# Optimization experiments

Hardware: AMD Instinct MI355X
Metric: run time of the kernel (lower is better)

The kernel has to match this reference:

```python
import jax, jax.numpy as jnp
import numpy as np

B, N, C = 8, 1025, 1024
H = 8
D = C // H  # 128
LORA = 16
TOK = 1024

def setup_inputs() -> dict:
    key = jax.random.key(0)
    ks = jax.random.split(key, 16)
    s = 0.02
    return {
        "x": jax.random.normal(ks[0], (B, N, C), jnp.float32),
        "style_k": jax.random.normal(ks[1], (B, N, C), jnp.float32),
        "style_v": jax.random.normal(ks[2], (B, N, C), jnp.float32),
        "W_qkv": jax.random.normal(ks[3], (C, 3 * C), jnp.float32) * s,
        "W_proj": jax.random.normal(ks[4], (C, C), jnp.float32) * s,
        "b_proj": jnp.zeros((C,), jnp.float32),
        "ak": jax.random.normal(ks[5], (TOK, LORA), jnp.float32) * s,
        "bk": jax.random.normal(ks[6], (LORA, C), jnp.float32) * s,
        "av": jax.random.normal(ks[7], (TOK, LORA), jnp.float32) * s,
        "bv": jax.random.normal(ks[8], (LORA, C), jnp.float32) * s,
        "W1": jax.random.normal(ks[9], (C, C // 4), jnp.float32) * s,
        "b1": jnp.zeros((C // 4,), jnp.float32),
        "W2": jax.random.normal(ks[10], (C // 4, 1), jnp.float32) * s,
        "b2": jnp.zeros((1,), jnp.float32),
    }

def reference(x, style_k, style_v, W_qkv, W_proj, b_proj, ak, bk, av, bv, W1, b1, W2, b2):
    Bx, Nx, Cx = x.shape
    # cls-token gating MLP over transposed patch tokens: cp has shape [B, C, N-1], N-1 == C
    cls_token = x[:, :1, :]                         # [B,1,C]
    cp = jnp.transpose(x[:, 1:, :], (0, 2, 1))      # [B,C,N-1]
    h = jax.nn.relu(cp @ W1 + b1)                   # [B,C,C//4]
    attn_w = jax.nn.sigmoid(h @ W2 + b2)            # [B,C,1]
    attn_w = attn_w[..., 0][:, None, :]             # [B,1,C]
    weighted_cls = cls_token * attn_w               # [B,1,C]

    qkv = (x @ W_qkv).reshape(Bx, Nx, 3, H, D)
    q, k, v = qkv[:, :, 0], qkv[:, :, 1], qkv[:, :, 2]  # each [B,N,H,D]

    tokens_k = ak @ bk                              # [TOK, C] (TOK == C)
    tokens_v = av @ bv
    lora_k = (style_k @ tokens_k.T).reshape(Bx, Nx, H, D)
    lora_v = (style_v @ tokens_v.T).reshape(Bx, Nx, H, D)

    kk = k + lora_k
    vv = v + lora_v
    scale = D ** -0.5  # xformers default softmax scale
    scores = jnp.einsum('bqhd,bkhd->bhqk', q, kk) * scale
    attn = jax.nn.softmax(scores, axis=-1)
    out = jnp.einsum('bhqk,bkhd->bqhd', attn, vv).reshape(Bx, Nx, Cx)
    out = out @ W_proj + b_proj

    x_return = jnp.concatenate([out[:, :1, :] + weighted_cls, out[:, 1:, :]], axis=1)
    return (x_return, vv)
```

## Files before the change

kernel.cpp:

```cpp
#include <hip/hip_runtime.h>
#include <hip/hip_bf16.h>
#include <stdint.h>

#define B_ 8
#define N_ 1025
#define C_ 1024
#define H_ 8
#define D_ 128
#define TOK_ 1024
#define LORA_ 16
#define M_ 8200
#define NPAD_ 1032

using bf16x8 = __attribute__((ext_vector_type(8))) short;
using f32x4  = __attribute__((ext_vector_type(4))) float;
typedef unsigned short u16;

__device__ __forceinline__ u16 f2bf(float f) {
    union { float f; unsigned u; } v; v.f = f;
    unsigned r = v.u + 0x7fffu + ((v.u >> 16) & 1u);
    return (u16)(r >> 16);
}

__device__ __forceinline__ void gload16(const u16* g, u16* l) {
    __builtin_amdgcn_global_load_lds(
        (const __attribute__((address_space(1))) void*)g,
        (__attribute__((address_space(3))) void*)l, 16, 0, 0);
}

__device__ __forceinline__ int xcd_swz(int bid, int nwg) {
    int cpx = nwg >> 3;
    return (bid & 7) * cpx + (bid >> 3);
}

__global__ __launch_bounds__(256) void cast3_kernel(
    const float* __restrict__ x, const float* __restrict__ sk, const float* __restrict__ sv,
    u16* __restrict__ xb, u16* __restrict__ skb, u16* __restrict__ svb)
{
    const float* in = blockIdx.y == 0 ? x : (blockIdx.y == 1 ? sk : sv);
    u16* out = blockIdx.y == 0 ? xb : (blockIdx.y == 1 ? skb : svb);
    size_t i = (size_t)blockIdx.x * 256 + threadIdx.x;
    float4 a = *((const float4*)in + i * 2);
    float4 b = *((const float4*)in + i * 2 + 1);
    bf16x8 v;
    v[0] = (short)f2bf(a.x); v[1] = (short)f2bf(a.y);
    v[2] = (short)f2bf(a.z); v[3] = (short)f2bf(a.w);
    v[4] = (short)f2bf(b.x); v[5] = (short)f2bf(b.y);
    v[6] = (short)f2bf(b.z); v[7] = (short)f2bf(b.w);
    *(bf16x8*)(out + i * 8) = v;
}

__global__ __launch_bounds__(256) void padcast16_kernel(
    const float* __restrict__ ak, const float* __restrict__ av,
    u16* __restrict__ akp, u16* __restrict__ avp)
{
    const float* in = blockIdx.y ? av : ak;
    u16* out = blockIdx.y ? avp : akp;
    int i = blockIdx.x * 256 + threadIdx.x;
    int t = i >> 4, l = i & 15;
    out[(size_t)t * 32 + l] = f2bf(in[i]);
    out[(size_t)t * 32 + 16 + l] = 0;
}

__global__ __launch_bounds__(256) void castb_kernel(
    const float* __restrict__ bk, const float* __restrict__ bv,
    u16* __restrict__ bkb, u16* __restrict__ bvb)
{
    const float* in = blockIdx.y ? bv : bk;
    u16* out = blockIdx.y ? bvb : bkb;
    int i = blockIdx.x * 256 + threadIdx.x;
    out[i] = f2bf(in[i]);
}

__global__ __launch_bounds__(256) void lora16_mfma(
    const u16* __restrict__ skb, const u16* __restrict__ svb,
    const u16* __restrict__ bkb, const u16* __restrict__ bvb,
    u16* __restrict__ sk16p, u16* __restrict__ sv16p)
{
    const u16* sb = blockIdx.y ? svb : skb;
    const u16* bb = blockIdx.y ? bvb : bkb;
    u16* op = blockIdx.y ? sv16p : sk16p;
    const int lane = threadIdx.x & 63, wid = threadIdx.x >> 6;
    const int base = blockIdx.x * 64 + wid * 16;
    int ma = base + (lane & 15); if (ma > M_ - 1) ma = M_ - 1;
    const int l = lane & 15;
    const u16* arow = sb + (size_t)ma * C_ + (lane >> 4) * 8;
    const u16* brow = bb + (size_t)l * C_ + (lane >> 4) * 8;
    f32x4 acc = {0.f, 0.f, 0.f, 0.f};
#pragma unroll
    for (int k0 = 0; k0 < C_; k0 += 32) {
        bf16x8 af = *(const bf16x8*)(arow + k0);
        bf16x8 bf = *(const bf16x8*)(brow + k0);
        acc = __builtin_amdgcn_mfma_f32_16x16x32_bf16(af, bf, acc, 0, 0, 0);
    }
#pragma unroll
    for (int r = 0; r < 4; ++r) {
        int m = base + (lane >> 4) * 4 + r; if (m > M_ - 1) m = M_ - 1;
        op[(size_t)m * 32 + l] = f2bf(acc[r]);
        op[(size_t)m * 32 + 16 + l] = 0;
    }
}

__global__ __launch_bounds__(256) void wt_kernel(
    const float* __restrict__ in, u16* __restrict__ out, int K, int Nw)
{
    __shared__ float t[32][33];
    int n0 = blockIdx.x * 32, k0 = blockIdx.y * 32;
    int tx = threadIdx.x & 31, ty = threadIdx.x >> 5;
#pragma unroll
    for (int yy = 0; yy < 32; yy += 8)
        t[ty + yy][tx] = in[(size_t)(k0 + ty + yy) * Nw + n0 + tx];
    __syncthreads();
#pragma unroll
    for (int yy = 0; yy < 32; yy += 8)
        out[(size_t)(n0 + ty + yy) * K + k0 + tx] = f2bf(t[tx][ty + yy]);
}

__global__ __launch_bounds__(256) void xt_kernel(
    const float* __restrict__ x, u16* __restrict__ xT)
{
    __shared__ float tb[32][33];
    int t0 = blockIdx.x * 32, c0 = blockIdx.y * 32, b = blockIdx.z;
    int tx = threadIdx.x & 31, ty = threadIdx.x >> 5;
#pragma unroll
    for (int yy = 0; yy < 32; yy += 8)
        tb[ty + yy][tx] = x[((size_t)b * N_ + 1 + t0 + ty + yy) * C_ + c0 + tx];
    __syncthreads();
#pragma unroll
    for (int yy = 0; yy < 32; yy += 8)
        xT[((size_t)b * 1024 + c0 + ty + yy) * 1024 + t0 + tx] = f2bf(tb[tx][ty + yy]);
}

__global__ __launch_bounds__(256) void vvt_kernel(
    const float* __restrict__ vv, u16* __restrict__ vvT)
{
    __shared__ float t[32][33];
    int n0 = blockIdx.x * 32, d0 = blockIdx.y * 32, bh = blockIdx.z;
    int b = bh >> 3, h = bh & 7;
    int tx = threadIdx.x & 31, ty = threadIdx.x >> 5;
#pragma unroll
    for (int yy = 0; yy < 32; yy += 8) {
        int n = n0 + ty + yy; if (n > 1024) n = 1024;
        t[ty + yy][tx] = vv[((size_t)(b * N_) + n) * C_ + h * D_ + d0 + tx];
    }
    __syncthreads();
#pragma unroll
    for (int yy = 0; yy < 32; yy += 8) {
        int n = n0 + tx;
        if (n < NPAD_)
            vvT[((size_t)bh * D_ + d0 + ty + yy) * NPAD_ + n] = f2bf(t[tx][ty + yy]);
    }
}

__device__ __forceinline__ void stage_tile(
    const u16* __restrict__ base, int row0, int maxrow,
    u16* lds, int k0, int lane, int wid)
{
#pragma unroll
    for (int j = 0; j < 4; ++j) {
        int i = wid * 4 + j;
        int p = i * 1024 + 16 * lane;
        int row = p >> 7, cb = p & 127;
        int cbs = cb ^ ((row & 7) << 4);
        int gr = row0 + row; if (gr > maxrow) gr = maxrow;
        gload16(base + (size_t)gr * 1024 + k0 + (cbs >> 1), lds + i * 512);
    }
}

__device__ __forceinline__ void gemm_pass(
    const u16* __restrict__ A, const u16* __restrict__ Bt, int row0, int nb0,
    u16* As, u16* Bs, f32x4 acc[4][4],
    const int lane, const int wid, const int wr, const int wc)
{
    for (int k0 = 0; k0 < 1024; k0 += 64) {
        __syncthreads();
        stage_tile(A,  row0, M_ - 1,    As, k0, lane, wid);
        stage_tile(Bt, nb0,  (1 << 30), Bs, k0, lane, wid);
        __syncthreads();
#pragma unroll
        for (int ks = 0; ks < 2; ++ks) {
            bf16x8 af[4], bfr[4];
#pragma unroll
            for (int mi = 0; mi < 4; ++mi) {
                int r = wr * 64 + mi * 16 + (lane & 15);
                int byte = (r * 128 + ks * 64 + (lane >> 4) * 16) ^ ((r & 7) << 4);
                af[mi] = *(const bf16x8*)((const char*)As + byte);
            }
#pragma unroll
            for (int ni = 0; ni < 4; ++ni) {
                int r = wc * 64 + ni * 16 + (lane & 15);
                int byte = (r * 128 + ks * 64 + (lane >> 4) * 16) ^ ((r & 7) << 4);
                bfr[ni] = *(const bf16x8*)((const char*)Bs + byte);
            }
#pragma unroll
            for (int mi = 0; mi < 4; ++mi)
#pragma unroll
                for (int ni = 0; ni < 4; ++ni)
                    acc[mi][ni] = __builtin_amdgcn_mfma_f32_16x16x32_bf16(
                        af[mi], bfr[ni], acc[mi][ni], 0, 0, 0);
        }
    }
}

__global__ __launch_bounds__(256) void se_gemm(
    const u16* __restrict__ xT, const u16* __restrict__ W1T,
    const float* __restrict__ b1, const float* __restrict__ W2,
    const float* __restrict__ b2, const float* __restrict__ x,
    float* __restrict__ wcls)
{
    __shared__ u16 As[8192], Bs[8192];
    __shared__ float red[128];
    const int tid = threadIdx.x, lane = tid & 63, wid = tid >> 6;
    const int wr = wid >> 1, wc = wid & 1;
    const int row0 = blockIdx.x * 128;
    if (tid < 128) red[tid] = 0.f;
    const f32x4 FZ = {0.f, 0.f, 0.f, 0.f};

#pragma unroll
    for (int pass = 0; pass < 2; ++pass) {
        f32x4 acc[4][4];
#pragma unroll
        for (int mi = 0; mi < 4; ++mi)
#pragma unroll
            for (int ni = 0; ni < 4; ++ni) acc[mi][ni] = FZ;
        gemm_pass(xT, W1T, row0, pass * 128, As, Bs, acc, lane, wid, wr, wc);
#pragma unroll
        for (int mi = 0; mi < 4; ++mi) {
#pragma unroll
            for (int r = 0; r < 4; ++r) {
                float v = 0.f;
#pragma unroll
                for (int ni = 0; ni < 4; ++ni) {
                    int j = pass * 128 + wc * 64 + ni * 16 + (lane & 15);
                    float h = acc[mi][ni][r] + b1[j];
                    v += fmaxf(h, 0.f) * W2[j];
                }
#pragma unroll
                for (int off = 1; off < 16; off <<= 1) v += __shfl_xor(v, off);
                if ((lane & 15) == 0)
                    atomicAdd(&red[wr * 64 + mi * 16 + (lane >> 4) * 4 + r], v);
            }
        }
    }
    __syncthreads();
    if (tid < 128) {
        int row = row0 + tid;
        int b = row >> 10, c = row & 1023;
        float aw = 1.f / (1.f + expf(-(red[tid] + b2[0])));
        wcls[row] = x[(size_t)b * N_ * C_ + c] * aw;
    }
}

__global__ __launch_bounds__(256) void qkv_gemm(
    const u16* __restrict__ xb, const u16* __restrict__ WqkvT,
    const u16* __restrict__ sk16p, const u16* __restrict__ sv16p,
    const u16* __restrict__ akp, const u16* __restrict__ avp,
    u16* __restrict__ qb, u16* __restrict__ kkb, float* __restrict__ vvout)
{
    __shared__ u16 As[8192], Bs[8192];
    const int tid = threadIdx.x, lane = tid & 63, wid = tid >> 6;
    const int wr = wid >> 1, wc = wid & 1;
    const int swz = xcd_swz(blockIdx.x, 65 * 24);
    const int row0 = (swz / 24) * 128;
    const int ct = swz % 24, region = ct >> 3;
    const int creg = (ct & 7) * 128;
    const f32x4 FZ = {0.f, 0.f, 0.f, 0.f};
    f32x4 acc[4][4];
#pragma unroll
    for (int mi = 0; mi < 4; ++mi)
#pragma unroll
        for (int ni = 0; ni < 4; ++ni) acc[mi][ni] = FZ;

    gemm_pass(xb, WqkvT, row0, ct * 128, As, Bs, acc, lane, wid, wr, wc);

    if (region >= 1) {
        const u16* a16 = (region == 1) ? sk16p : sv16p;
        const u16* b16 = (region == 1) ? akp : avp;
        bf16x8 af2[4], bf2v[4];
#pragma unroll
        for (int mi = 0; mi < 4; ++mi) {
            int gr = row0 + wr * 64 + mi * 16 + (lane & 15);
            if (gr > M_ - 1) gr = M_ - 1;
            af2[mi] = *(const bf16x8*)(a16 + (size_t)gr * 32 + (lane >> 4) * 8);
        }
#pragma unroll
        for (int ni = 0; ni < 4; ++ni) {
            int gc = creg + wc * 64 + ni * 16 + (lane & 15);
            bf2v[ni] = *(const bf16x8*)(b16 + (size_t)gc * 32 + (lane >> 4) * 8);
        }
#pragma unroll
        for (int mi = 0; mi < 4; ++mi)
#pragma unroll
            for (int ni = 0; ni < 4; ++ni)
                acc[mi][ni] = __builtin_amdgcn_mfma_f32_16x16x32_bf16(
                    af2[mi], bf2v[ni], acc[mi][ni], 0, 0, 0);
    }

#pragma unroll
    for (int mi = 0; mi < 4; ++mi) {
#pragma unroll
        for (int r = 0; r < 4; ++r) {
            int gr = row0 + wr * 64 + mi * 16 + (lane >> 4) * 4 + r;
            if (gr >= M_) continue;
#pragma unroll
            for (int ni = 0; ni < 4; ++ni) {
                int gc = creg + wc * 64 + ni * 16 + (lane & 15);
                float v = acc[mi][ni][r];
                if (region == 0)      qb [(size_t)gr * C_ + gc] = f2bf(v);
                else if (region == 1) kkb[(size_t)gr * C_ + gc] = f2bf(v);
                else                  vvout[(size_t)gr * C_ + gc] = v;
            }
        }
    }
}

__global__ __launch_bounds__(256) void proj_gemm(
    const u16* __restrict__ ob, const u16* __restrict__ WprojT,
    const float* __restrict__ bias, const float* __restrict__ wcls,
    float* __restrict__ outp)
{
    __shared__ u16 As[8192], Bs[8192];
    const int tid = threadIdx.x, lane = tid & 63, wid = tid >> 6;
    const int wr = wid >> 1, wc = wid & 1;
    const int swz = xcd_swz(blockIdx.x, 65 * 8);
    const int row0 = (swz / 8) * 128;
    const int ct = swz % 8;
    const f32x4 FZ = {0.f, 0.f, 0.f, 0.f};
    f32x4 acc[4][4];
#pragma unroll
    for (int mi = 0; mi < 4; ++mi)
#pragma unroll
        for (int ni = 0; ni < 4; ++ni) acc[mi][ni] = FZ;

    gemm_pass(ob, WprojT, row0, ct * 128, As, Bs, acc, lane, wid, wr, wc);

#pragma unroll
    for (int mi = 0; mi < 4; ++mi) {
#pragma unroll
        for (int r = 0; r < 4; ++r) {
            int gr = row0 + wr * 64 + mi * 16 + (lane >> 4) * 4 + r;
            if (gr >= M_) continue;
#pragma unroll
            for (int ni = 0; ni < 4; ++ni) {
                int gc = ct * 128 + wc * 64 + ni * 16 + (lane & 15);
                float v = acc[mi][ni][r] + bias[gc];
                if (gr % N_ == 0) v += wcls[(gr / N_) * C_ + gc];
                outp[(size_t)gr * C_ + gc] = v;
            }
        }
    }
}

__device__ __forceinline__ void attn_stage(
    const u16* __restrict__ kbase, const u16* __restrict__ vbase,
    u16* Ksb, u16* Vsb, int kv0, int lane, int wid)
{
#pragma unroll
    for (int j = 0; j < 4; ++j) {
        int i = wid * 4 + j;
        int p = i * 1024 + 16 * lane;
        int row = p >> 8, cb = p & 255;
        int cbs = cb ^ ((row & 7) << 4);
        int n = kv0 + row; if (n > 1024) n = 1024;
        gload16(kbase + (size_t)n * C_ + (cbs >> 1), Ksb + i * 512);
    }
#pragma unroll
    for (int j = 0; j < 4; ++j) {
        int i = wid * 4 + j;
        int p = i * 1024 + 16 * lane;
        int row = p >> 7, cb = p & 127;
        int cbs = cb ^ ((row & 7) << 4);
        int st = kv0 + (cbs >> 1); if (st > NPAD_ - 8) st = NPAD_ - 8;
        gload16(vbase + (size_t)row * NPAD_ + st, Vsb + i * 512);
    }
}

__global__ __launch_bounds__(256) void attn_kernel(
    const u16* __restrict__ qb, const u16* __restrict__ kkb,
    const u16* __restrict__ vvT, u16* __restrict__ ob)
{
    __shared__ u16 Ks[2][8192];
    __shared__ u16 Vs[2][8192];
    __shared__ u16 Ps[4096];
    const int tid = threadIdx.x, lane = tid & 63, wid = tid >> 6;
    const int swz = xcd_swz(blockIdx.x, 17 * 64);
    const int qt = swz % 17, bh = swz / 17, b = bh >> 3, h = bh & 7;
    const int n0q = qt * 64;
    const float SCALE = 0.08838834764831845f;
    const u16* kbase = kkb + (size_t)b * N_ * C_ + h * D_;
    const u16* vbase = vvT + (size_t)bh * D_ * NPAD_;

    bf16x8 qf[4];
    {
        int qrow = n0q + wid * 16 + (lane & 15); if (qrow > 1024) qrow = 1024;
        const u16* qbase = qb + (size_t)(b * N_ + qrow) * C_ + h * D_ + (lane >> 4) * 8;
#pragma unroll
        for (int ks = 0; ks < 4; ++ks) qf[ks] = *(const bf16x8*)(qbase + ks * 32);
    }

    const bf16x8 ones = {0x3F80, 0x3F80, 0x3F80, 0x3F80, 0x3F80, 0x3F80, 0x3F80, 0x3F80};
    float mrow[4];
    const f32x4 FZ = {0.f, 0.f, 0.f, 0.f};
    f32x4 of[8], lsacc = FZ;
#pragma unroll
    for (int r = 0; r < 4; ++r) mrow[r] = -3e38f;
#pragma unroll
    for (int ct = 0; ct < 8; ++ct) of[ct] = FZ;

    char* psb = (char*)Ps + wid * 2048;

    attn_stage(kbase, vbase, Ks[0], Vs[0], 0, lane, wid);

    for (int t = 0; t < 17; ++t) {
        const int cur = t & 1;
        const int kv0 = t * 64;
        __syncthreads();
        if (t < 16)
            attn_stage(kbase, vbase, Ks[cur ^ 1], Vs[cur ^ 1], (t + 1) * 64, lane, wid);

        f32x4 s[4];
        __builtin_amdgcn_s_setprio(1);
#pragma unroll
        for (int jt = 0; jt < 4; ++jt) {
            f32x4 a = FZ;
#pragma unroll
            for (int ks = 0; ks < 4; ++ks) {
                int kvr = jt * 16 + (lane & 15);
                int byte = (kvr * 256 + ks * 64 + (lane >> 4) * 16) ^ ((kvr & 7) << 4);
                bf16x8 kf = *(const bf16x8*)((const char*)Ks[cur] + byte);
                a = __builtin_amdgcn_mfma_f32_16x16x32_bf16(qf[ks], kf, a, 0, 0, 0);
            }
            s[jt] = a;
        }
        __builtin_amdgcn_s_setprio(0);
#pragma unroll
        for (int jt = 0; jt < 4; ++jt) {
            f32x4 a = s[jt] * SCALE;
            int kvglob = kv0 + jt * 16 + (lane & 15);
            if (kvglob > 1024) { a[0] = -3e38f; a[1] = -3e38f; a[2] = -3e38f; a[3] = -3e38f; }
            s[jt] = a;
        }

        float tm[4];
        int need = 0;
#pragma unroll
        for (int r = 0; r < 4; ++r) {
            float t0 = fmaxf(fmaxf(s[0][r], s[1][r]), fmaxf(s[2][r], s[3][r]));
#pragma unroll
            for (int off = 1; off < 16; off <<= 1) t0 = fmaxf(t0, __shfl_xor(t0, off));
            tm[r] = t0;
            need |= (t0 > mrow[r] + 8.f) ? 1 : 0;
        }
        if (__any(need)) {
            float al[4];
#pragma unroll
            for (int r = 0; r < 4; ++r) {
                float mn = fmaxf(mrow[r], tm[r]);
                al[r] = __expf(mrow[r] - mn);
                mrow[r] = mn;
            }
#pragma unroll
            for (int ct = 0; ct < 8; ++ct)
#pragma unroll
                for (int r = 0; r < 4; ++r) of[ct][r] *= al[r];
#pragma unroll
            for (int r = 0; r < 4; ++r) lsacc[r] *= al[r];
        }
#pragma unroll
        for (int jt = 0; jt < 4; ++jt)
#pragma unroll
            for (int r = 0; r < 4; ++r) s[jt][r] = __expf(s[jt][r] - mrow[r]);

#pragma unroll
        for (int jt = 0; jt < 4; ++jt)
#pragma unroll
            for (int r = 0; r < 4; ++r) {
                int pr = (lane >> 4) * 4 + r;
                int byte = (pr * 128 + (jt * 16 + (lane & 15)) * 2) ^ ((pr & 7) << 4);
                *(u16*)(psb + byte) = f2bf(s[jt][r]);
            }

        bf16x8 pa[2];
#pragma unroll
        for (int ks2 = 0; ks2 < 2; ++ks2) {
            int prr = lane & 15;
            int byte = (prr * 128 + ks2 * 64 + (lane >> 4) * 16) ^ ((prr & 7) << 4);
            pa[ks2] = *(const bf16x8*)(psb + byte);
        }
        __builtin_amdgcn_s_setprio(1);
        lsacc = __builtin_amdgcn_mfma_f32_16x16x32_bf16(pa[0], ones, lsacc, 0, 0, 0);
        lsacc = __builtin_amdgcn_mfma_f32_16x16x32_bf16(pa[1], ones, lsacc, 0, 0, 0);
#pragma unroll
        for (int ct = 0; ct < 8; ++ct)
#pragma unroll
            for (int ks2 = 0; ks2 < 2; ++ks2) {
                int d = ct * 16 + (lane & 15);
                int byte = (d * 128 + ks2 * 64 + (lane >> 4) * 16) ^ ((d & 7) << 4);
                bf16x8 vf = *(const bf16x8*)((const char*)Vs[cur] + byte);
                of[ct] = __builtin_amdgcn_mfma_f32_16x16x32_bf16(pa[ks2], vf, of[ct], 0, 0, 0);
            }
        __builtin_amdgcn_s_setprio(0);
    }

#pragma unroll
    for (int ct = 0; ct < 8; ++ct)
#pragma unroll
        for (int r = 0; r < 4; ++r) {
            int n = n0q + wid * 16 + (lane >> 4) * 4 + r;
            if (n <= 1024)
                ob[(size_t)(b * N_ + n) * C_ + h * D_ + ct * 16 + (lane & 15)] =
                    f2bf(of[ct][r] / lsacc[r]);
        }
}

extern "C" void kernel_launch(void* const* d_in, const int* in_sizes, int n_in,
                              void* d_out, int out_size, void* d_ws, size_t ws_size,
                              hipStream_t stream)
{
    const float* x       = (const float*)d_in[0];
    const float* style_k = (const float*)d_in[1];
    const float* style_v = (const float*)d_in[2];
    const float* W_qkv   = (const float*)d_in[3];
    const float* W_proj  = (const float*)d_in[4];
    const float* b_proj  = (const float*)d_in[5];
    const float* ak      = (const float*)d_in[6];
    const float* bk      = (const float*)d_in[7];
    const float* av      = (const float*)d_in[8];
    const float* bv      = (const float*)d_in[9];
    const float* W1      = (const float*)d_in[10];
    const float* b1      = (const float*)d_in[11];
    const float* W2      = (const float*)d_in[12];
    const float* b2      = (const float*)d_in[13];

    float* outp   = (float*)d_out;
    float* vv_out = outp + (size_t)M_ * C_;

    u16* WqkvT = (u16*)outp;
    u16* xbb   = WqkvT + (size_t)3072 * 1024;
    u16* W1T   = xbb + (size_t)M_ * C_;
    u16* akp   = W1T + (size_t)256 * 1024;
    u16* avp   = akp + 1024 * 32;
    u16* bkb   = avp + 1024 * 32;
    u16* bvb   = bkb + 16 * 1024;
    u16* sk16p = bvb + 16 * 1024;
    u16* sv16p = sk16p + (size_t)M_ * 32;

    u16* ws     = (u16*)d_ws;
    u16* qb     = ws;
    u16* kkb    = qb  + (size_t)M_ * C_;
    u16* obuf   = kkb + (size_t)M_ * C_;
    u16* vvT    = obuf + (size_t)M_ * C_;
    u16* WprojT = vvT + (size_t)B_ * H_ * D_ * NPAD_;
    float* wcls = (float*)(WprojT + (size_t)1024 * 1024);
    u16* skb = obuf;
    u16* svb = vvT;
    u16* xT  = qb;

    wt_kernel<<<dim3(96, 32), 256, 0, stream>>>(W_qkv, WqkvT, 1024, 3072);
    wt_kernel<<<dim3(32, 32), 256, 0, stream>>>(W_proj, WprojT, 1024, 1024);
    wt_kernel<<<dim3(8, 32), 256, 0, stream>>>(W1, W1T, 1024, 256);
    padcast16_kernel<<<dim3(64, 2), 256, 0, stream>>>(ak, av, akp, avp);
    castb_kernel<<<dim3(64, 2), 256, 0, stream>>>(bk, bv, bkb, bvb);
    cast3_kernel<<<dim3(4100, 3), 256, 0, stream>>>(x, style_k, style_v, xbb, skb, svb);
    xt_kernel<<<dim3(32, 32, 8), 256, 0, stream>>>(x, xT);
    se_gemm<<<dim3(64), 256, 0, stream>>>(xT, W1T, b1, W2, b2, x, wcls);
    lora16_mfma<<<dim3(129, 2), 256, 0, stream>>>(skb, svb, bkb, bvb, sk16p, sv16p);

    qkv_gemm<<<dim3(65 * 24), 256, 0, stream>>>(xbb, WqkvT, sk16p, sv16p, akp, avp,
                                                qb, kkb, vv_out);
    vvt_kernel<<<dim3(33, 4, 64), 256, 0, stream>>>(vv_out, vvT);
    attn_kernel<<<dim3(17 * 64), 256, 0, stream>>>(qb, kkb, vvT, obuf);
    proj_gemm<<<dim3(65 * 8), 256, 0, stream>>>(obuf, WprojT, b_proj, wcls, outp);
}
```

Baseline: 361.1 us.

## Split K/V staging with single V buffer, exp2 softmax, packed bf16 convert

Attention K and V loads are split. K stays double-buffered and is prefetched one tile ahead, while V moves to a single buffer loaded at the start of each iteration. A second barrier with partial vmcnt waits before the PV MFMAs, so the V load overlaps the QK and softmax work. Softmax now uses exp2 with log2e folded into the scale and a matching rescale threshold, and P is converted with the packed v_cvt_pk_bf16_f32 instruction. This cuts LDS use, which may raise occupancy, at the cost of an extra barrier per tile and V-load latency sitting closer to its use.

```diff
diff --git a/kernel.cpp b/kernel.cpp
--- a/kernel.cpp
+++ b/kernel.cpp
@@ -20,6 +20,12 @@
     union { float f; unsigned u; } v; v.f = f;
     unsigned r = v.u + 0x7fffu + ((v.u >> 16) & 1u);
     return (u16)(r >> 16);
+}
+
+__device__ __forceinline__ unsigned cvt_pk_bf16(float lo, float hi) {
+    unsigned r;
+    asm("v_cvt_pk_bf16_f32 %0, %1, %2" : "=v"(r) : "v"(lo), "v"(hi));
+    return r;
 }
 
 __device__ __forceinline__ void gload16(const u16* g, u16* l) {
@@ -351,9 +357,8 @@
     }
 }
 
-__device__ __forceinline__ void attn_stage(
-    const u16* __restrict__ kbase, const u16* __restrict__ vbase,
-    u16* Ksb, u16* Vsb, int kv0, int lane, int wid)
+__device__ __forceinline__ void stageK(
+    const u16* __restrict__ kbase, u16* Ksb, int kv0, int lane, int wid)
 {
 #pragma unroll
     for (int j = 0; j < 4; ++j) {
@@ -364,6 +369,10 @@
         int n = kv0 + row; if (n > 1024) n = 1024;
         gload16(kbase + (size_t)n * C_ + (cbs >> 1), Ksb + i * 512);
     }
+}
+__device__ __forceinline__ void stageV(
+    const u16* __restrict__ vbase, u16* Vsb, int kv0, int lane, int wid)
+{
 #pragma unroll
     for (int j = 0; j < 4; ++j) {
         int i = wid * 4 + j;
@@ -380,13 +389,13 @@
     const u16* __restrict__ vvT, u16* __restrict__ ob)
 {
     __shared__ u16 Ks[2][8192];
-    __shared__ u16 Vs[2][8192];
+    __shared__ u16 Vs[8192];
     __shared__ u16 Ps[4096];
     const int tid = threadIdx.x, lane = tid & 63, wid = tid >> 6;
     const int swz = xcd_swz(blockIdx.x, 17 * 64);
     const int qt = swz % 17, bh = swz / 17, b = bh >> 3, h = bh & 7;
     const int n0q = qt * 64;
-    const float SCALE = 0.08838834764831845f;
+    const float C2 = 0.1275006182f;
     const u16* kbase = kkb + (size_t)b * N_ * C_ + h * D_;
     const u16* vbase = vvT + (size_t)bh * D_ * NPAD_;
 
@@ -409,14 +418,16 @@
 
     char* psb = (char*)Ps + wid * 2048;
 
-    attn_stage(kbase, vbase, Ks[0], Vs[0], 0, lane, wid);
+    stageK(kbase, Ks[0], 0, lane, wid);
 
     for (int t = 0; t < 17; ++t) {
         const int cur = t & 1;
         const int kv0 = t * 64;
-        __syncthreads();
-        if (t < 16)
-            attn_stage(kbase, vbase, Ks[cur ^ 1], Vs[cur ^ 1], (t + 1) * 64, lane, wid);
+        asm volatile("s_waitcnt vmcnt(0)" ::: "memory");
+        __builtin_amdgcn_s_barrier();
+        __builtin_amdgcn_sched_barrier(0);
+        stageV(vbase, Vs, kv0, lane, wid);
+        if (t < 16) stageK(kbase, Ks[cur ^ 1], kv0 + 64, lane, wid);
 
         f32x4 s[4];
         __builtin_amdgcn_s_setprio(1);
@@ -435,7 +446,7 @@
         __builtin_amdgcn_s_setprio(0);
 #pragma unroll
         for (int jt = 0; jt < 4; ++jt) {
-            f32x4 a = s[jt] * SCALE;
+            f32x4 a = s[jt] * C2;
             int kvglob = kv0 + jt * 16 + (lane & 15);
             if (kvglob > 1024) { a[0] = -3e38f; a[1] = -3e38f; a[2] = -3e38f; a[3] = -3e38f; }
             s[jt] = a;
@@ -449,14 +460,14 @@
 #pragma unroll
             for (int off = 1; off < 16; off <<= 1) t0 = fmaxf(t0, __shfl_xor(t0, off));
             tm[r] = t0;
-            need |= (t0 > mrow[r] + 8.f) ? 1 : 0;
+            need |= (t0 > mrow[r] + 11.54f) ? 1 : 0;
         }
         if (__any(need)) {
             float al[4];
 #pragma unroll
             for (int r = 0; r < 4; ++r) {
                 float mn = fmaxf(mrow[r], tm[r]);
-                al[r] = __expf(mrow[r] - mn);
+                al[r] = exp2f(mrow[r] - mn);
                 mrow[r] = mn;
             }
 #pragma unroll
@@ -469,16 +480,19 @@
 #pragma unroll
         for (int jt = 0; jt < 4; ++jt)
 #pragma unroll
-            for (int r = 0; r < 4; ++r) s[jt][r] = __expf(s[jt][r] - mrow[r]);
-
-#pragma unroll
-        for (int jt = 0; jt < 4; ++jt)
-#pragma unroll
-            for (int r = 0; r < 4; ++r) {
-                int pr = (lane >> 4) * 4 + r;
-                int byte = (pr * 128 + (jt * 16 + (lane & 15)) * 2) ^ ((pr & 7) << 4);
-                *(u16*)(psb + byte) = f2bf(s[jt][r]);
-            }
+            for (int r = 0; r < 4; ++r) s[jt][r] = exp2f(s[jt][r] - mrow[r]);
+
+#pragma unroll
+        for (int jt = 0; jt < 4; ++jt) {
+            unsigned pk01 = cvt_pk_bf16(s[jt][0], s[jt][1]);
+            unsigned pk23 = cvt_pk_bf16(s[jt][2], s[jt][3]);
+            int colb = (jt * 16 + (lane & 15)) * 2;
+            int pr0 = (lane >> 4) * 4;
+            *(u16*)(psb + ((pr0 * 128 + colb) ^ ((pr0 & 7) << 4)))           = (u16)pk01;
+            *(u16*)(psb + (((pr0 + 1) * 128 + colb) ^ (((pr0 + 1) & 7) << 4))) = (u16)(pk01 >> 16);
+            *(u16*)(psb + (((pr0 + 2) * 128 + colb) ^ (((pr0 + 2) & 7) << 4))) = (u16)pk23;
+            *(u16*)(psb + (((pr0 + 3) * 128 + colb) ^ (((pr0 + 3) & 7) << 4))) = (u16)(pk23 >> 16);
+        }
 
         bf16x8 pa[2];
 #pragma unroll
@@ -487,6 +501,12 @@
             int byte = (prr * 128 + ks2 * 64 + (lane >> 4) * 16) ^ ((prr & 7) << 4);
             pa[ks2] = *(const bf16x8*)(psb + byte);
         }
+
+        if (t < 16) asm volatile("s_waitcnt vmcnt(4)" ::: "memory");
+        else        asm volatile("s_waitcnt vmcnt(0)" ::: "memory");
+        __builtin_amdgcn_s_barrier();
+        __builtin_amdgcn_sched_barrier(0);
+
         __builtin_amdgcn_s_setprio(1);
         lsacc = __builtin_amdgcn_mfma_f32_16x16x32_bf16(pa[0], ones, lsacc, 0, 0, 0);
         lsacc = __builtin_amdgcn_mfma_f32_16x16x32_bf16(pa[1], ones, lsacc, 0, 0, 0);
@@ -496,7 +516,7 @@
             for (int ks2 = 0; ks2 < 2; ++ks2) {
                 int d = ct * 16 + (lane & 15);
                 int byte = (d * 128 + ks2 * 64 + (lane >> 4) * 16) ^ ((d & 7) << 4);
-                bf16x8 vf = *(const bf16x8*)((const char*)Vs[cur] + byte);
+                bf16x8 vf = *(const bf16x8*)((const char*)Vs + byte);
                 of[ct] = __builtin_amdgcn_mfma_f32_16x16x32_bf16(pa[ks2], vf, of[ct], 0, 0, 0);
             }
         __builtin_amdgcn_s_setprio(0);
```

New measurement: 365.7 us. About the same (+1.3%).
